# Optimization experiments

Hardware: AMD Instinct MI355X
Metric: run time of the kernel (lower is better)

Reference implementation:

```python
import jax, jax.numpy as jnp
import numpy as np

B, T, N, C = 32, 12, 1024, 2   # batch, lookback window, n_series, in_channels
D, H, K, OUT = 16, 64, 2, 12   # embedding_dim, rnn_units, cheb_k, out_dim (horizon)


def setup_inputs() -> dict:
    key = jax.random.key(0)
    ks = jax.random.split(key, 12)
    p = lambda k, sh, s=0.1: jax.random.normal(k, sh, dtype=jnp.float32) * s
    return {
        "source": jax.random.normal(ks[0], (B, T, N, C), dtype=jnp.float32),
        "node_emb": p(ks[1], (N, D), 0.3),
        # layer 0: dim_in = C + H
        "gate_w0": p(ks[2], (D, K, C + H, 2 * H)),
        "gate_b0": p(ks[3], (D, 2 * H)),
        "upd_w0": p(ks[4], (D, K, C + H, H)),
        "upd_b0": p(ks[5], (D, H)),
        # layer 1: dim_in = H + H
        "gate_w1": p(ks[6], (D, K, 2 * H, 2 * H)),
        "gate_b1": p(ks[7], (D, 2 * H)),
        "upd_w1": p(ks[8], (D, K, 2 * H, H)),
        "upd_b1": p(ks[9], (D, H)),
        # end_conv: Conv2d(1, OUT*out_channels, kernel=(1,H)) == linear over hidden dim
        "conv_w": p(ks[10], (OUT, H)),
        "conv_b": p(ks[11], (OUT,)),
    }


def _supports(node_emb):
    # softmax(relu(E E^T)) row-normalized adaptive adjacency; Chebyshev stack (K, N, N)
    A = jax.nn.softmax(jax.nn.relu(node_emb @ node_emb.T), axis=1)
    s = [jnp.eye(N, dtype=A.dtype), A]
    for _ in range(2, K):
        s.append(2.0 * A @ s[-1] - s[-2])
    return jnp.stack(s, axis=0)


def _gcn(x, node_emb, w_pool, b_pool, supports):
    # x: (B, N, Cin); per-node adaptive weights from pools
    w = jnp.einsum('nd,dkio->nkio', node_emb, w_pool)     # (N, K, Cin, Cout)
    b = node_emb @ b_pool                                 # (N, Cout)
    xg = jnp.einsum('knm,bmc->bnkc', supports, x)         # (B, N, K, Cin)
    return jnp.einsum('bnki,nkio->bno', xg, w) + b


def _layer(x_seq, node_emb, supports, gw, gb, uw, ub):
    # x_seq: (B, T, N, Cin) -> (B, T, N, H) via GRU-style AGCRN cell, scanned over T
    def step(state, x_t):
        inp = jnp.concatenate([x_t, state], axis=-1)
        zr = jax.nn.sigmoid(_gcn(inp, node_emb, gw, gb, supports))
        z, r = jnp.split(zr, 2, axis=-1)
        cand = jnp.concatenate([x_t, z * state], axis=-1)
        hc = jnp.tanh(_gcn(cand, node_emb, uw, ub, supports))
        h = r * state + (1.0 - r) * hc
        return h, h

    init = jnp.zeros((x_seq.shape[0], N, H), dtype=x_seq.dtype)
    _, hs = jax.lax.scan(step, init, jnp.swapaxes(x_seq, 0, 1))
    return jnp.swapaxes(hs, 0, 1)


def reference(source, node_emb, gate_w0, gate_b0, upd_w0, upd_b0,
              gate_w1, gate_b1, upd_w1, upd_b1, conv_w, conv_b,
              teacher_forcing_ratio=0):
    sup = _supports(node_emb)  # adaptive supports depend only on static node_emb
    h1 = _layer(source, node_emb, sup, gate_w0, gate_b0, upd_w0, upd_b0)
    h2 = _layer(h1, node_emb, sup, gate_w1, gate_b1, upd_w1, upd_b1)
    last = h2[:, -1]  # (B, N, H)
    # end_conv over hidden dim -> (B, OUT, N); out_channels==1 so squeeze folds away
    out = jnp.einsum('bnh,oh->bon', last, conv_w) + conv_b[None, :, None]
    return out
```

## Files before the change

kernel.cpp:

```cpp
#include <hip/hip_runtime.h>
#include <hip/hip_fp16.h>


typedef _Float16 f16x8 __attribute__((ext_vector_type(8)));
typedef _Float16 f16x2 __attribute__((ext_vector_type(2)));
typedef float f32x4 __attribute__((ext_vector_type(4)));

__global__ __launch_bounds__(256) void compute_A_kernel(const float* __restrict__ E,
                                                        __half* __restrict__ Ah) {
  int n = blockIdx.x;
  int tid = threadIdx.x;
  __shared__ float red[256];
  float en[16];
#pragma unroll
  for (int d = 0; d < 16; ++d) en[d] = E[n * 16 + d];
  float v[4];
#pragma unroll
  for (int q = 0; q < 4; ++q) {
    int m = tid + q * 256;
    const float* Em = E + m * 16;
    float dot = 0.f;
#pragma unroll
    for (int d = 0; d < 16; ++d) dot += en[d] * Em[d];
    v[q] = fmaxf(dot, 0.f);
  }
  float mx = fmaxf(fmaxf(v[0], v[1]), fmaxf(v[2], v[3]));
  red[tid] = mx; __syncthreads();
  for (int s = 128; s > 0; s >>= 1) { if (tid < s) red[tid] = fmaxf(red[tid], red[tid + s]); __syncthreads(); }
  mx = red[0];
  __syncthreads();
  float e[4], sum = 0.f;
#pragma unroll
  for (int q = 0; q < 4; ++q) { e[q] = expf(v[q] - mx); sum += e[q]; }
  red[tid] = sum; __syncthreads();
  for (int s = 128; s > 0; s >>= 1) { if (tid < s) red[tid] += red[tid + s]; __syncthreads(); }
  float inv = 1.f / red[0];
#pragma unroll
  for (int q = 0; q < 4; ++q) Ah[(size_t)n * 1024 + tid + q * 256] = __float2half(e[q] * inv);
}

__global__ void pool_transpose_all_kernel(const float* __restrict__ gw0, const float* __restrict__ uw0,
                                          const float* __restrict__ gw1, const float* __restrict__ uw1,
                                          float* __restrict__ poolT) {
  int t = blockIdx.x * 256 + threadIdx.x;
  if (t >= 1277952) return;
  const float* pool; int F, Fp, O, loc;
  if (t < 327680)       { pool = gw0; F = 66;  Fp = 80;  O = 128; loc = t; }
  else if (t < 491520)  { pool = uw0; F = 66;  Fp = 80;  O = 64;  loc = t - 327680; }
  else if (t < 1015808) { pool = gw1; F = 128; Fp = 128; O = 128; loc = t - 491520; }
  else                  { pool = uw1; F = 128; Fp = 128; O = 64;  loc = t - 1015808; }
  int KIp = 2 * Fp;
  int kip = loc % KIp;
  int rest = loc / KIp;
  int o = rest % O;
  int d = rest / O;
  int kk = (kip >= Fp) ? 1 : 0;
  int j = kip - kk * Fp;
  int i;
  if (F == Fp) i = j;
  else i = (j < 64) ? j + 2 : (j < 66 ? j - 64 : -1);
  poolT[t] = (i >= 0) ? pool[(((size_t)d * 2 + kk) * F + i) * O + o] : 0.f;
}

__global__ __launch_bounds__(256) void make_wt_all_kernel(
    const float* __restrict__ E, const float* __restrict__ poolT,
    __half* __restrict__ WtG0, __half* __restrict__ WtU0,
    __half* __restrict__ WtG1, __half* __restrict__ WtU1) {
  __shared__ float Es[64 * 17];
  __shared__ __align__(16) _Float16 wbuf[64][264];
  int bx = blockIdx.x;
  int o, O, KIp; const float* pt; __half* Wt;
  if (bx < 128)      { o = bx;       O = 128; KIp = 160; pt = poolT;           Wt = WtG0; }
  else if (bx < 192) { o = bx - 128; O = 64;  KIp = 160; pt = poolT + 327680;  Wt = WtU0; }
  else if (bx < 320) { o = bx - 192; O = 128; KIp = 256; pt = poolT + 491520;  Wt = WtG1; }
  else               { o = bx - 320; O = 64;  KIp = 256; pt = poolT + 1015808; Wt = WtU1; }
  int n0 = blockIdx.y * 64;
  {
    int nl = threadIdx.x >> 2, d0 = (threadIdx.x & 3) * 4;
    float4 v = *(const float4*)(E + (size_t)(n0 + nl) * 16 + d0);
    Es[nl * 17 + d0 + 0] = v.x; Es[nl * 17 + d0 + 1] = v.y;
    Es[nl * 17 + d0 + 2] = v.z; Es[nl * 17 + d0 + 3] = v.w;
  }
  __syncthreads();
  int nl = threadIdx.x & 63;
  int q = KIp >> 2;
  int ku = __builtin_amdgcn_readfirstlane((threadIdx.x >> 6) * q);
  float e[16];
#pragma unroll
  for (int d = 0; d < 16; ++d) e[d] = Es[nl * 17 + d];
  const float* pbase = pt + (size_t)o * KIp + ku;
  int strideOK = O * KIp;
  for (int kk = 0; kk < q; kk += 8) {
    float a[8] = {0.f, 0.f, 0.f, 0.f, 0.f, 0.f, 0.f, 0.f};
#pragma unroll
    for (int d = 0; d < 16; ++d) {
      const float* pd = pbase + (size_t)d * strideOK + kk;
#pragma unroll
      for (int j = 0; j < 8; ++j) a[j] = fmaf(e[d], pd[j], a[j]);
    }
    f16x8 pk;
#pragma unroll
    for (int j = 0; j < 8; ++j) pk[j] = (_Float16)a[j];
    *(f16x8*)&wbuf[nl][ku + kk] = pk;
  }
  __syncthreads();
  int chunks = KIp >> 3;
  int tot = 64 * chunks;
  for (int idx = threadIdx.x; idx < tot; idx += 256) {
    int nsub = idx / chunks;
    int pos = (idx - nsub * chunks) * 8;
    *(float4*)(Wt + ((size_t)(n0 + nsub) * O + o) * KIp + pos) = *(float4*)&wbuf[nsub][pos];
  }
}

__global__ void make_b_all_kernel(const float* __restrict__ E,
                                  const float* __restrict__ gb0, const float* __restrict__ ub0,
                                  const float* __restrict__ gb1, const float* __restrict__ ub1,
                                  float* __restrict__ Bg0, float* __restrict__ Bu0,
                                  float* __restrict__ Bg1, float* __restrict__ Bu1) {
  int tid = blockIdx.x * 256 + threadIdx.x;
  if (tid >= 1024 * 384) return;
  int n = tid / 384, c = tid - n * 384;
  const float* pool; float* outp; int O, o;
  if (c < 128)      { pool = gb0; outp = Bg0; O = 128; o = c; }
  else if (c < 192) { pool = ub0; outp = Bu0; O = 64;  o = c - 128; }
  else if (c < 320) { pool = gb1; outp = Bg1; O = 128; o = c - 192; }
  else              { pool = ub1; outp = Bu1; O = 64;  o = c - 320; }
  const float* En = E + n * 16;
  float a = 0.f;
#pragma unroll
  for (int d = 0; d < 16; ++d) a += En[d] * pool[d * O + o];
  outp[n * O + o] = a;
}

__global__ void zero_kernel(float* __restrict__ p, int count) {
  int i = blockIdx.x * 256 + threadIdx.x;
  if (i < count) p[i] = 0.f;
}

__global__ void build_x16_kernel(const float* __restrict__ src, __half* __restrict__ x16) {
  int bid = blockIdx.x; int t = bid >> 5, b = bid & 31;
  const float* s = src + (size_t)(b * 12 + t) * 2048;
  __half* dst = x16 + t * 64 + b * 2;
  for (int n = threadIdx.x; n < 1024; n += 256) {
    float2 v = *(const float2*)(s + n * 2);
    *(__half2*)(dst + (size_t)n * 768) = __floats2half2_rn(v.x, v.y);
  }
}

__global__ __launch_bounds__(256) void gemm_nt_kernel(
    const __half* __restrict__ Ahg, const __half* __restrict__ X0g,
    const __half* __restrict__ X1g, __half* __restrict__ Yg,
    int Nc, int cstride, int split) {
  __shared__ __align__(16) _Float16 As[64][72];
  __shared__ __align__(16) _Float16 Bs[64][80];
  const _Float16* __restrict__ Ah = (const _Float16*)Ahg;
  _Float16* __restrict__ Y = (_Float16*)Yg;
  int tid = threadIdx.x;
  int row0 = blockIdx.y * 64;
  int col0 = blockIdx.x * 64;
  const _Float16* __restrict__ Xsrc =
      (col0 < split) ? (const _Float16*)X0g : (const _Float16*)X1g;
  int colg = (col0 < split) ? col0 : col0 - split;
  int wave = tid >> 6, lane = tid & 63;
  int wm = wave & 1, wn = wave >> 1;
  int fm = lane & 15, fg = lane >> 4;

  int sr = tid >> 2, sc = (tid & 3) * 16;
  const _Float16* pa = Ah + (size_t)(row0 + sr) * 1024 + sc;
  int kp = tid & 31, cg = tid >> 5;
  const _Float16* pb0 = Xsrc + (size_t)(2 * kp) * cstride + colg + cg * 8;
  const _Float16* pb1 = pb0 + cstride;

  f16x8 ra0 = *(const f16x8*)(pa);
  f16x8 ra1 = *(const f16x8*)(pa + 8);
  f16x8 rb0 = *(const f16x8*)(pb0);
  f16x8 rb1 = *(const f16x8*)(pb1);

  int kk = 2 * kp;
  int kchunk = kp >> 2;
  int kin = kk & 7;
  f32x4 acc[2][2] = {};
  for (int k0 = 0; k0 < 1024; k0 += 64) {
    *(f16x8*)&As[sr][sc] = ra0;
    *(f16x8*)&As[sr][sc + 8] = ra1;
#pragma unroll
    for (int i = 0; i < 8; ++i) {
      int c = cg * 8 + i;
      f16x2 p; p[0] = rb0[i]; p[1] = rb1[i];
      int pos = ((kchunk ^ (c & 7)) << 3) + kin;
      *(f16x2*)&Bs[c][pos] = p;
    }
    __syncthreads();
    if (k0 + 64 < 1024) {
      ra0 = *(const f16x8*)(pa + k0 + 64);
      ra1 = *(const f16x8*)(pa + k0 + 72);
      rb0 = *(const f16x8*)(pb0 + (size_t)(k0 + 64) * cstride);
      rb1 = *(const f16x8*)(pb1 + (size_t)(k0 + 64) * cstride);
    }
#pragma unroll
    for (int kc = 0; kc < 2; ++kc) {
      int ck = kc * 4 + fg;
      f16x8 af[2], bf[2];
#pragma unroll
      for (int i = 0; i < 2; ++i)
        af[i] = *(const f16x8*)&As[wm * 32 + i * 16 + fm][kc * 32 + fg * 8];
#pragma unroll
      for (int j = 0; j < 2; ++j) {
        int cl = wn * 32 + j * 16 + fm;
        bf[j] = *(const f16x8*)&Bs[cl][(ck ^ (cl & 7)) << 3];
      }
#pragma unroll
      for (int i = 0; i < 2; ++i)
#pragma unroll
        for (int j = 0; j < 2; ++j)
          acc[i][j] = __builtin_amdgcn_mfma_f32_16x16x32_f16(af[i], bf[j], acc[i][j], 0, 0, 0);
    }
    __syncthreads();
  }
#pragma unroll
  for (int i = 0; i < 2; ++i) {
#pragma unroll
    for (int j = 0; j < 2; ++j) {
      int col = col0 + wn * 32 + j * 16 + fm;
      int rbase = row0 + wm * 32 + i * 16 + fg * 4;
#pragma unroll
      for (int r = 0; r < 4; ++r)
        Y[(size_t)(rbase + r) * Nc + col] = (_Float16)acc[i][j][r];
    }
  }
}

__global__ __launch_bounds__(256) void gate0_kernel(
    const __half* __restrict__ h16, const __half* __restrict__ YB,
    const float* __restrict__ src, const __half* __restrict__ Axt, int tstep,
    const __half* __restrict__ Wtg, const float* __restrict__ Bg,
    const float* __restrict__ h32, __half* __restrict__ zh, float* __restrict__ rbuf) {
  constexpr int KIP = 160, STRIDE = 168;
  __shared__ __align__(16) _Float16 Xs[32 * STRIDE];
  int n = blockIdx.x;
  int t = threadIdx.x;
#pragma unroll
  for (int u = 0; u < 2; ++u) {
    int idx = t + u * 256;
    int b = idx >> 4, part = (idx >> 3) & 1, ch = idx & 7;
    const _Float16* s = part ? (const _Float16*)YB + (size_t)n * 2048 + b * 64 + ch * 8
                             : (const _Float16*)h16 + (size_t)n * 2048 + b * 64 + ch * 8;
    *(f16x8*)&Xs[b * STRIDE + part * 80 + ch * 8] = *(const f16x8*)s;
  }
  if (t < 32) {
    int b = t;
    float2 xv = *(const float2*)(src + ((size_t)(b * 12 + tstep) * 1024 + n) * 2);
    Xs[b * STRIDE + 64] = (_Float16)xv.x;
    Xs[b * STRIDE + 65] = (_Float16)xv.y;
    const _Float16* ax = (const _Float16*)Axt + (size_t)n * 768 + tstep * 64 + b * 2;
    Xs[b * STRIDE + 144] = ax[0];
    Xs[b * STRIDE + 145] = ax[1];
  }
  for (int idx = t; idx < 896; idx += 256) {
    int b = idx / 28, jj = idx % 28;
    int col = (jj < 14) ? 66 + jj : 132 + jj;
    Xs[b * STRIDE + col] = (_Float16)0.f;
  }
  __syncthreads();
  int wave = t >> 6, lane = t & 63;
  int fm = lane & 15, fg = lane >> 4;
  f32x4 acc[2][2] = {};
  const _Float16* Wn = (const _Float16*)Wtg + ((size_t)n * 128 + wave * 32) * KIP;
#pragma unroll
  for (int kc = 0; kc < KIP / 32; ++kc) {
    f16x8 af[2], bf[2];
#pragma unroll
    for (int i = 0; i < 2; ++i)
      af[i] = *(const f16x8*)&Xs[(i * 16 + fm) * STRIDE + kc * 32 + fg * 8];
#pragma unroll
    for (int j = 0; j < 2; ++j)
      bf[j] = *(const f16x8*)(Wn + (size_t)(j * 16 + fm) * KIP + kc * 32 + fg * 8);
#pragma unroll
    for (int i = 0; i < 2; ++i)
#pragma unroll
      for (int j = 0; j < 2; ++j)
        acc[i][j] = __builtin_amdgcn_mfma_f32_16x16x32_f16(af[i], bf[j], acc[i][j], 0, 0, 0);
  }
  const float* Bn = Bg + n * 128;
#pragma unroll
  for (int j = 0; j < 2; ++j) {
    int o = wave * 32 + j * 16 + fm;
    float bias = Bn[o];
#pragma unroll
    for (int i = 0; i < 2; ++i)
#pragma unroll
      for (int r = 0; r < 4; ++r) {
        int b = i * 16 + fg * 4 + r;
        float s = 1.f / (1.f + __expf(-(acc[i][j][r] + bias)));
        size_t base = (size_t)n * 2048 + b * 64;
        if (o < 64) zh[base + o] = __float2half(s * h32[base + o]);
        else        rbuf[base + o - 64] = s;
      }
  }
}

__global__ __launch_bounds__(256) void upd0_kernel(
    const __half* __restrict__ zh, const __half* __restrict__ YA2,
    const float* __restrict__ src, const __half* __restrict__ Axt, int tstep,
    const __half* __restrict__ Wtg, const float* __restrict__ Bu,
    const float* __restrict__ rbuf, float* __restrict__ h32, __half* __restrict__ h16) {
  constexpr int KIP = 160, STRIDE = 168;
  __shared__ __align__(16) _Float16 Xs[32 * STRIDE];
  int n = blockIdx.x;
  int t = threadIdx.x;
#pragma unroll
  for (int u = 0; u < 2; ++u) {
    int idx = t + u * 256;
    int b = idx >> 4, part = (idx >> 3) & 1, ch = idx & 7;
    const _Float16* s = part ? (const _Float16*)YA2 + (size_t)n * 4096 + b * 64 + ch * 8
                             : (const _Float16*)zh + (size_t)n * 2048 + b * 64 + ch * 8;
    *(f16x8*)&Xs[b * STRIDE + part * 80 + ch * 8] = *(const f16x8*)s;
  }
  if (t < 32) {
    int b = t;
    float2 xv = *(const float2*)(src + ((size_t)(b * 12 + tstep) * 1024 + n) * 2);
    Xs[b * STRIDE + 64] = (_Float16)xv.x;
    Xs[b * STRIDE + 65] = (_Float16)xv.y;
    const _Float16* ax = (const _Float16*)Axt + (size_t)n * 768 + tstep * 64 + b * 2;
    Xs[b * STRIDE + 144] = ax[0];
    Xs[b * STRIDE + 145] = ax[1];
  }
  for (int idx = t; idx < 896; idx += 256) {
    int b = idx / 28, jj = idx % 28;
    int col = (jj < 14) ? 66 + jj : 132 + jj;
    Xs[b * STRIDE + col] = (_Float16)0.f;
  }
  __syncthreads();
  int wave = t >> 6, lane = t & 63;
  int fm = lane & 15, fg = lane >> 4;
  f32x4 acc[2] = {};
  const _Float16* Wn = (const _Float16*)Wtg + ((size_t)n * 64 + wave * 16) * KIP;
#pragma unroll
  for (int kc = 0; kc < KIP / 32; ++kc) {
    f16x8 bf = *(const f16x8*)(Wn + (size_t)fm * KIP + kc * 32 + fg * 8);
#pragma unroll
    for (int i = 0; i < 2; ++i) {
      f16x8 af = *(const f16x8*)&Xs[(i * 16 + fm) * STRIDE + kc * 32 + fg * 8];
      acc[i] = __builtin_amdgcn_mfma_f32_16x16x32_f16(af, bf, acc[i], 0, 0, 0);
    }
  }
  int o = wave * 16 + fm;
  float bias = Bu[n * 64 + o];
#pragma unroll
  for (int i = 0; i < 2; ++i)
#pragma unroll
    for (int r = 0; r < 4; ++r) {
      int b = i * 16 + fg * 4 + r;
      float x = acc[i][r] + bias;
      x = fminf(fmaxf(x, -15.f), 15.f);
      float e = __expf(2.f * x);
      float hc = (e - 1.f) / (e + 1.f);
      size_t base = (size_t)n * 2048 + b * 64;
      float rr = rbuf[base + o];
      float hnew = rr * h32[base + o] + (1.f - rr) * hc;
      h32[base + o] = hnew;
      h16[base + o] = __float2half(hnew);
    }
}

__global__ __launch_bounds__(256) void gate1_kernel(
    const __half* __restrict__ h1_16, const __half* __restrict__ h2_16,
    const __half* __restrict__ YB, const __half* __restrict__ YA2,
    const __half* __restrict__ Wtg, const float* __restrict__ Bg,
    const float* __restrict__ h32, __half* __restrict__ zh, float* __restrict__ rbuf) {
  constexpr int KIP = 256, STRIDE = 264;
  __shared__ __align__(16) _Float16 Xs[32 * STRIDE];
  int n = blockIdx.x;
  int t = threadIdx.x;
#pragma unroll
  for (int u = 0; u < 4; ++u) {
    int idx = t + u * 256;
    int b = idx >> 5, q = idx & 31;
    const _Float16* s;
    if (q < 8)       s = (const _Float16*)h1_16 + (size_t)n * 2048 + b * 64 + q * 8;
    else if (q < 16) s = (const _Float16*)h2_16 + (size_t)n * 2048 + b * 64 + (q - 8) * 8;
    else if (q < 24) s = (const _Float16*)YB + (size_t)n * 2048 + b * 64 + (q - 16) * 8;
    else             s = (const _Float16*)YA2 + (size_t)n * 4096 + 2048 + b * 64 + (q - 24) * 8;
    *(f16x8*)&Xs[b * STRIDE + q * 8] = *(const f16x8*)s;
  }
  __syncthreads();
  int wave = t >> 6, lane = t & 63;
  int fm = lane & 15, fg = lane >> 4;
  f32x4 acc[2][2] = {};
  const _Float16* Wn = (const _Float16*)Wtg + ((size_t)n * 128 + wave * 32) * KIP;
#pragma unroll
  for (int kc = 0; kc < KIP / 32; ++kc) {
    f16x8 af[2], bf[2];
#pragma unroll
    for (int i = 0; i < 2; ++i)
      af[i] = *(const f16x8*)&Xs[(i * 16 + fm) * STRIDE + kc * 32 + fg * 8];
#pragma unroll
    for (int j = 0; j < 2; ++j)
      bf[j] = *(const f16x8*)(Wn + (size_t)(j * 16 + fm) * KIP + kc * 32 + fg * 8);
#pragma unroll
    for (int i = 0; i < 2; ++i)
#pragma unroll
      for (int j = 0; j < 2; ++j)
        acc[i][j] = __builtin_amdgcn_mfma_f32_16x16x32_f16(af[i], bf[j], acc[i][j], 0, 0, 0);
  }
  const float* Bn = Bg + n * 128;
#pragma unroll
  for (int j = 0; j < 2; ++j) {
    int o = wave * 32 + j * 16 + fm;
    float bias = Bn[o];
#pragma unroll
    for (int i = 0; i < 2; ++i)
#pragma unroll
      for (int r = 0; r < 4; ++r) {
        int b = i * 16 + fg * 4 + r;
        float s = 1.f / (1.f + __expf(-(acc[i][j][r] + bias)));
        size_t base = (size_t)n * 2048 + b * 64;
        if (o < 64) zh[base + o] = __float2half(s * h32[base + o]);
        else        rbuf[base + o - 64] = s;
      }
  }
}

__global__ __launch_bounds__(256) void upd1_kernel(
    const __half* __restrict__ h1_16, const __half* __restrict__ zh,
    const __half* __restrict__ YB, const __half* __restrict__ YC,
    const __half* __restrict__ Wtg, const float* __restrict__ Bu,
    const float* __restrict__ rbuf, float* __restrict__ h32, __half* __restrict__ h16) {
  constexpr int KIP = 256, STRIDE = 264;
  __shared__ __align__(16) _Float16 Xs[32 * STRIDE];
  int n = blockIdx.x;
  int t = threadIdx.x;
#pragma unroll
  for (int u = 0; u < 4; ++u) {
    int idx = t + u * 256;
    int b = idx >> 5, q = idx & 31;
    const _Float16* s;
    if (q < 8)       s = (const _Float16*)h1_16 + (size_t)n * 2048 + b * 64 + q * 8;
    else if (q < 16) s = (const _Float16*)zh + (size_t)n * 2048 + b * 64 + (q - 8) * 8;
    else if (q < 24) s = (const _Float16*)YB + (size_t)n * 2048 + b * 64 + (q - 16) * 8;
    else             s = (const _Float16*)YC + (size_t)n * 2048 + b * 64 + (q - 24) * 8;
    *(f16x8*)&Xs[b * STRIDE + q * 8] = *(const f16x8*)s;
  }
  __syncthreads();
  int wave = t >> 6, lane = t & 63;
  int fm = lane & 15, fg = lane >> 4;
  f32x4 acc[2] = {};
  const _Float16* Wn = (const _Float16*)Wtg + ((size_t)n * 64 + wave * 16) * KIP;
#pragma unroll
  for (int kc = 0; kc < KIP / 32; ++kc) {
    f16x8 bf = *(const f16x8*)(Wn + (size_t)fm * KIP + kc * 32 + fg * 8);
#pragma unroll
    for (int i = 0; i < 2; ++i) {
      f16x8 af = *(const f16x8*)&Xs[(i * 16 + fm) * STRIDE + kc * 32 + fg * 8];
      acc[i] = __builtin_amdgcn_mfma_f32_16x16x32_f16(af, bf, acc[i], 0, 0, 0);
    }
  }
  int o = wave * 16 + fm;
  float bias = Bu[n * 64 + o];
#pragma unroll
  for (int i = 0; i < 2; ++i)
#pragma unroll
    for (int r = 0; r < 4; ++r) {
      int b = i * 16 + fg * 4 + r;
      float x = acc[i][r] + bias;
      x = fminf(fmaxf(x, -15.f), 15.f);
      float e = __expf(2.f * x);
      float hc = (e - 1.f) / (e + 1.f);
      size_t base = (size_t)n * 2048 + b * 64;
      float rr = rbuf[base + o];
      float hnew = rr * h32[base + o] + (1.f - rr) * hc;
      h32[base + o] = hnew;
      h16[base + o] = __float2half(hnew);
    }
}

__global__ void final_conv_kernel(const float* __restrict__ h2, const float* __restrict__ cw,
                                  const float* __restrict__ cb, float* __restrict__ out) {
  int tid = blockIdx.x * 256 + threadIdx.x;
  if (tid >= 32 * 1024) return;
  int n = tid & 1023, b = tid >> 10;
  const float* hp = h2 + ((size_t)n * 32 + b) * 64;
  float hv[64];
#pragma unroll
  for (int i = 0; i < 64; ++i) hv[i] = hp[i];
#pragma unroll
  for (int o = 0; o < 12; ++o) {
    float acc = cb[o];
#pragma unroll
    for (int i = 0; i < 64; ++i) acc += hv[i] * cw[o * 64 + i];
    out[((size_t)b * 12 + o) * 1024 + n] = acc;
  }
}

extern "C" void kernel_launch(void* const* d_in, const int* in_sizes, int n_in,
                              void* d_out, int out_size, void* d_ws, size_t ws_size,
                              hipStream_t stream) {
  const float* src = (const float*)d_in[0];
  const float* E   = (const float*)d_in[1];
  const float* gw0 = (const float*)d_in[2];
  const float* gb0 = (const float*)d_in[3];
  const float* uw0 = (const float*)d_in[4];
  const float* ub0 = (const float*)d_in[5];
  const float* gw1 = (const float*)d_in[6];
  const float* gb1 = (const float*)d_in[7];
  const float* uw1 = (const float*)d_in[8];
  const float* ub1 = (const float*)d_in[9];
  const float* cw  = (const float*)d_in[10];
  const float* cb  = (const float*)d_in[11];
  float* out = (float*)d_out;
  (void)in_sizes; (void)n_in; (void)out_size; (void)ws_size;

  char* base = (char*)d_ws;
  size_t off = 0;
  auto alloc = [&](size_t bytes) -> void* {
    void* p = base + off; off += (bytes + 511) & ~(size_t)511; return p;
  };
  __half* Ah   = (__half*)alloc((size_t)1024 * 1024 * 2);
  __half* WtG0 = (__half*)alloc((size_t)1024 * 128 * 160 * 2);
  __half* WtU0 = (__half*)alloc((size_t)1024 * 64 * 160 * 2);
  __half* WtG1 = (__half*)alloc((size_t)1024 * 128 * 256 * 2);
  __half* WtU1 = (__half*)alloc((size_t)1024 * 64 * 256 * 2);
  float*  Bg0  = (float*) alloc((size_t)1024 * 128 * 4);
  float*  Bu0  = (float*) alloc((size_t)1024 * 64 * 4);
  float*  Bg1  = (float*) alloc((size_t)1024 * 128 * 4);
  float*  Bu1  = (float*) alloc((size_t)1024 * 64 * 4);
  float*  h1_32 = (float*)alloc((size_t)1024 * 2048 * 4);
  float*  h2_32 = (float*)alloc((size_t)1024 * 2048 * 4);
  __half* h1_16 = (__half*)alloc((size_t)1024 * 2048 * 2);
  __half* h2_16 = (__half*)alloc((size_t)1024 * 2048 * 2);
  __half* YB   = (__half*)alloc((size_t)1024 * 2048 * 2);
  __half* zh   = (__half*)alloc((size_t)1024 * 2048 * 2);
  __half* YA2  = (__half*)alloc((size_t)1024 * 4096 * 2);
  __half* YC   = (__half*)alloc((size_t)1024 * 2048 * 2);
  __half* Axt  = (__half*)alloc((size_t)1024 * 768 * 2);
  float*  rbuf = (float*) alloc((size_t)1024 * 2048 * 4);
  float*  poolT = rbuf;
  __half* x16  = (__half*)(rbuf + (size_t)1310720);

  compute_A_kernel<<<1024, 256, 0, stream>>>(E, Ah);
  pool_transpose_all_kernel<<<(1277952 + 255) / 256, 256, 0, stream>>>(gw0, uw0, gw1, uw1, poolT);
  make_wt_all_kernel<<<dim3(384, 16), 256, 0, stream>>>(E, poolT, WtG0, WtU0, WtG1, WtU1);
  make_b_all_kernel<<<(1024 * 384 + 255) / 256, 256, 0, stream>>>(E, gb0, ub0, gb1, ub1,
                                                                  Bg0, Bu0, Bg1, Bu1);
  build_x16_kernel<<<384, 256, 0, stream>>>(src, x16);
  gemm_nt_kernel<<<dim3(12, 16), 256, 0, stream>>>(Ah, (__half*)x16, (__half*)x16, Axt,
                                                   768, 768, 768);
  zero_kernel<<<(7340032 + 255) / 256, 256, 0, stream>>>(h1_32, 7340032);

  for (int t = 0; t < 12; ++t) {
    gate0_kernel<<<1024, 256, 0, stream>>>(h1_16, YB, src, Axt, t, WtG0, Bg0, h1_32, zh, rbuf);
    gemm_nt_kernel<<<dim3(64, 16), 256, 0, stream>>>(Ah, zh, h2_16, YA2, 4096, 2048, 2048);
    upd0_kernel<<<1024, 256, 0, stream>>>(zh, YA2, src, Axt, t, WtU0, Bu0, rbuf, h1_32, h1_16);
    gemm_nt_kernel<<<dim3(32, 16), 256, 0, stream>>>(Ah, h1_16, h1_16, YB, 2048, 2048, 2048);
    gate1_kernel<<<1024, 256, 0, stream>>>(h1_16, h2_16, YB, YA2, WtG1, Bg1, h2_32, zh, rbuf);
    gemm_nt_kernel<<<dim3(32, 16), 256, 0, stream>>>(Ah, zh, zh, YC, 2048, 2048, 2048);
    upd1_kernel<<<1024, 256, 0, stream>>>(h1_16, zh, YB, YC, WtU1, Bu1, rbuf, h2_32, h2_16);
  }

  final_conv_kernel<<<(32 * 1024 + 255) / 256, 256, 0, stream>>>(h2_32, cw, cb, out);
}
```

Measured before the change: 1.523 ms.

## Compute per-node weights with MFMA and double K-tile depth in support GEMM

The per-node weight generation (E times weight pools) moves from scalar FP32 FMAs to an MFMA GEMM. E and the transposed pools are converted to fp16 and zero-padded along D to 32 first. Separately, the support GEMM now stages 128-wide K tiles per iteration instead of 64, which halves the barrier count and raises the bytes loaded per sync, at the cost of more LDS and registers. Computing the weights with fp16 inputs reduces their precision.

```diff
diff --git a/kernel.cpp b/kernel.cpp
--- a/kernel.cpp
+++ b/kernel.cpp
@@ -3,7 +3,7 @@
 
 
 typedef _Float16 f16x8 __attribute__((ext_vector_type(8)));
-typedef _Float16 f16x2 __attribute__((ext_vector_type(2)));
+typedef _Float16 f16x4 __attribute__((ext_vector_type(4)));
 typedef float f32x4 __attribute__((ext_vector_type(4)));
 
 __global__ __launch_bounds__(256) void compute_A_kernel(const float* __restrict__ E,
@@ -39,77 +39,81 @@
   for (int q = 0; q < 4; ++q) Ah[(size_t)n * 1024 + tid + q * 256] = __float2half(e[q] * inv);
 }
 
-__global__ void pool_transpose_all_kernel(const float* __restrict__ gw0, const float* __restrict__ uw0,
-                                          const float* __restrict__ gw1, const float* __restrict__ uw1,
-                                          float* __restrict__ poolT) {
+__global__ void build_e16_kernel(const float* __restrict__ E, __half* __restrict__ E16) {
   int t = blockIdx.x * 256 + threadIdx.x;
-  if (t >= 1277952) return;
+  if (t >= 1024 * 32) return;
+  int d = t & 31;
+  E16[t] = (d < 16) ? __float2half(E[(t >> 5) * 16 + d]) : __half(0);
+}
+
+__global__ void pool_t16_kernel(const float* __restrict__ gw0, const float* __restrict__ uw0,
+                                const float* __restrict__ gw1, const float* __restrict__ uw1,
+                                __half* __restrict__ poolT16) {
+  int t = blockIdx.x * 256 + threadIdx.x;
+  if (t >= 79872 * 32) return;
+  int d = t & 31, j = t >> 5;
+  if (d >= 16) { poolT16[t] = __half(0); return; }
   const float* pool; int F, Fp, O, loc;
-  if (t < 327680)       { pool = gw0; F = 66;  Fp = 80;  O = 128; loc = t; }
-  else if (t < 491520)  { pool = uw0; F = 66;  Fp = 80;  O = 64;  loc = t - 327680; }
-  else if (t < 1015808) { pool = gw1; F = 128; Fp = 128; O = 128; loc = t - 491520; }
-  else                  { pool = uw1; F = 128; Fp = 128; O = 64;  loc = t - 1015808; }
+  if (j < 20480)      { pool = gw0; F = 66;  Fp = 80;  O = 128; loc = j; }
+  else if (j < 30720) { pool = uw0; F = 66;  Fp = 80;  O = 64;  loc = j - 20480; }
+  else if (j < 63488) { pool = gw1; F = 128; Fp = 128; O = 128; loc = j - 30720; }
+  else                { pool = uw1; F = 128; Fp = 128; O = 64;  loc = j - 63488; }
   int KIp = 2 * Fp;
-  int kip = loc % KIp;
-  int rest = loc / KIp;
-  int o = rest % O;
-  int d = rest / O;
+  int o = loc / KIp, kip = loc - o * KIp;
   int kk = (kip >= Fp) ? 1 : 0;
-  int j = kip - kk * Fp;
+  int jj = kip - kk * Fp;
   int i;
-  if (F == Fp) i = j;
-  else i = (j < 64) ? j + 2 : (j < 66 ? j - 64 : -1);
-  poolT[t] = (i >= 0) ? pool[(((size_t)d * 2 + kk) * F + i) * O + o] : 0.f;
-}
-
-__global__ __launch_bounds__(256) void make_wt_all_kernel(
-    const float* __restrict__ E, const float* __restrict__ poolT,
+  if (F == Fp) i = jj;
+  else i = (jj < 64) ? jj + 2 : (jj < 66 ? jj - 64 : -1);
+  poolT16[t] = (i >= 0) ? __float2half(pool[(((size_t)d * 2 + kk) * F + i) * O + o]) : __half(0);
+}
+
+__global__ __launch_bounds__(256) void make_wt_mfma_kernel(
+    const __half* __restrict__ E16g, const __half* __restrict__ poolT16g,
     __half* __restrict__ WtG0, __half* __restrict__ WtU0,
     __half* __restrict__ WtG1, __half* __restrict__ WtU1) {
-  __shared__ float Es[64 * 17];
+  __shared__ __align__(16) _Float16 Es[64][40];
   __shared__ __align__(16) _Float16 wbuf[64][264];
+  const _Float16* E16 = (const _Float16*)E16g;
+  const _Float16* pT = (const _Float16*)poolT16g;
   int bx = blockIdx.x;
-  int o, O, KIp; const float* pt; __half* Wt;
-  if (bx < 128)      { o = bx;       O = 128; KIp = 160; pt = poolT;           Wt = WtG0; }
-  else if (bx < 192) { o = bx - 128; O = 64;  KIp = 160; pt = poolT + 327680;  Wt = WtU0; }
-  else if (bx < 320) { o = bx - 192; O = 128; KIp = 256; pt = poolT + 491520;  Wt = WtG1; }
-  else               { o = bx - 320; O = 64;  KIp = 256; pt = poolT + 1015808; Wt = WtU1; }
+  __half* Wt; int OK, jbase;
+  if (bx < 80)       { Wt = WtG0; OK = 128 * 160; jbase = bx * 256; }
+  else if (bx < 120) { Wt = WtU0; OK = 64 * 160;  jbase = (bx - 80) * 256; }
+  else if (bx < 248) { Wt = WtG1; OK = 128 * 256; jbase = (bx - 120) * 256; }
+  else               { Wt = WtU1; OK = 64 * 256;  jbase = (bx - 248) * 256; }
+  int jglob0 = bx * 256;
   int n0 = blockIdx.y * 64;
   {
-    int nl = threadIdx.x >> 2, d0 = (threadIdx.x & 3) * 4;
-    float4 v = *(const float4*)(E + (size_t)(n0 + nl) * 16 + d0);
-    Es[nl * 17 + d0 + 0] = v.x; Es[nl * 17 + d0 + 1] = v.y;
-    Es[nl * 17 + d0 + 2] = v.z; Es[nl * 17 + d0 + 3] = v.w;
-  }
-  __syncthreads();
-  int nl = threadIdx.x & 63;
-  int q = KIp >> 2;
-  int ku = __builtin_amdgcn_readfirstlane((threadIdx.x >> 6) * q);
-  float e[16];
-#pragma unroll
-  for (int d = 0; d < 16; ++d) e[d] = Es[nl * 17 + d];
-  const float* pbase = pt + (size_t)o * KIp + ku;
-  int strideOK = O * KIp;
-  for (int kk = 0; kk < q; kk += 8) {
-    float a[8] = {0.f, 0.f, 0.f, 0.f, 0.f, 0.f, 0.f, 0.f};
-#pragma unroll
-    for (int d = 0; d < 16; ++d) {
-      const float* pd = pbase + (size_t)d * strideOK + kk;
-#pragma unroll
-      for (int j = 0; j < 8; ++j) a[j] = fmaf(e[d], pd[j], a[j]);
-    }
-    f16x8 pk;
-#pragma unroll
-    for (int j = 0; j < 8; ++j) pk[j] = (_Float16)a[j];
-    *(f16x8*)&wbuf[nl][ku + kk] = pk;
-  }
-  __syncthreads();
-  int chunks = KIp >> 3;
-  int tot = 64 * chunks;
-  for (int idx = threadIdx.x; idx < tot; idx += 256) {
-    int nsub = idx / chunks;
-    int pos = (idx - nsub * chunks) * 8;
-    *(float4*)(Wt + ((size_t)(n0 + nsub) * O + o) * KIp + pos) = *(float4*)&wbuf[nsub][pos];
+    int r = threadIdx.x >> 2, ch = (threadIdx.x & 3) * 8;
+    *(f16x8*)&Es[r][ch] = *(const f16x8*)(E16 + (size_t)(n0 + r) * 32 + ch);
+  }
+  __syncthreads();
+  int wave = threadIdx.x >> 6, lane = threadIdx.x & 63;
+  int fm = lane & 15, fg = lane >> 4;
+  f16x8 af[4];
+#pragma unroll
+  for (int i = 0; i < 4; ++i) af[i] = *(const f16x8*)&Es[i * 16 + fm][fg * 8];
+  f32x4 acc[4][4] = {};
+#pragma unroll
+  for (int j = 0; j < 4; ++j) {
+    int jc = jglob0 + wave * 64 + j * 16 + fm;
+    f16x8 bf = *(const f16x8*)(pT + (size_t)jc * 32 + fg * 8);
+#pragma unroll
+    for (int i = 0; i < 4; ++i)
+      acc[i][j] = __builtin_amdgcn_mfma_f32_16x16x32_f16(af[i], bf, acc[i][j], 0, 0, 0);
+  }
+#pragma unroll
+  for (int i = 0; i < 4; ++i)
+#pragma unroll
+    for (int j = 0; j < 4; ++j)
+#pragma unroll
+      for (int r = 0; r < 4; ++r)
+        wbuf[i * 16 + fg * 4 + r][wave * 64 + j * 16 + fm] = (_Float16)acc[i][j][r];
+  __syncthreads();
+  for (int idx = threadIdx.x; idx < 64 * 32; idx += 256) {
+    int nsub = idx >> 5, pos = (idx & 31) * 8;
+    *(float4*)(Wt + (size_t)(n0 + nsub) * OK + jbase + pos) = *(float4*)&wbuf[nsub][pos];
   }
 }
 
@@ -152,8 +156,8 @@
     const __half* __restrict__ Ahg, const __half* __restrict__ X0g,
     const __half* __restrict__ X1g, __half* __restrict__ Yg,
     int Nc, int cstride, int split) {
-  __shared__ __align__(16) _Float16 As[64][72];
-  __shared__ __align__(16) _Float16 Bs[64][80];
+  __shared__ __align__(16) _Float16 As[64][136];
+  __shared__ __align__(16) _Float16 Bs[64][144];
   const _Float16* __restrict__ Ah = (const _Float16*)Ahg;
   _Float16* __restrict__ Y = (_Float16*)Yg;
   int tid = threadIdx.x;
@@ -166,40 +170,41 @@
   int wm = wave & 1, wn = wave >> 1;
   int fm = lane & 15, fg = lane >> 4;
 
-  int sr = tid >> 2, sc = (tid & 3) * 16;
+  int sr = tid >> 2, sc = (tid & 3) * 32;
   const _Float16* pa = Ah + (size_t)(row0 + sr) * 1024 + sc;
-  int kp = tid & 31, cg = tid >> 5;
-  const _Float16* pb0 = Xsrc + (size_t)(2 * kp) * cstride + colg + cg * 8;
-  const _Float16* pb1 = pb0 + cstride;
-
-  f16x8 ra0 = *(const f16x8*)(pa);
-  f16x8 ra1 = *(const f16x8*)(pa + 8);
-  f16x8 rb0 = *(const f16x8*)(pb0);
-  f16x8 rb1 = *(const f16x8*)(pb1);
-
-  int kk = 2 * kp;
-  int kchunk = kp >> 2;
-  int kin = kk & 7;
+  int kq = tid & 31, cg = tid >> 5;
+  int kb = 4 * kq;
+  const _Float16* pb = Xsrc + (size_t)kb * cstride + colg + cg * 8;
+  int chunk = kq >> 1;
+  int kin = (kq & 1) * 4;
+
+  f16x8 ra[4], rb[4];
+#pragma unroll
+  for (int c = 0; c < 4; ++c) ra[c] = *(const f16x8*)(pa + c * 8);
+#pragma unroll
+  for (int r = 0; r < 4; ++r) rb[r] = *(const f16x8*)(pb + (size_t)r * cstride);
+
   f32x4 acc[2][2] = {};
-  for (int k0 = 0; k0 < 1024; k0 += 64) {
-    *(f16x8*)&As[sr][sc] = ra0;
-    *(f16x8*)&As[sr][sc + 8] = ra1;
+  for (int k0 = 0; k0 < 1024; k0 += 128) {
+#pragma unroll
+    for (int c = 0; c < 4; ++c) *(f16x8*)&As[sr][sc + c * 8] = ra[c];
 #pragma unroll
     for (int i = 0; i < 8; ++i) {
       int c = cg * 8 + i;
-      f16x2 p; p[0] = rb0[i]; p[1] = rb1[i];
-      int pos = ((kchunk ^ (c & 7)) << 3) + kin;
-      *(f16x2*)&Bs[c][pos] = p;
+      f16x4 p;
+      p[0] = rb[0][i]; p[1] = rb[1][i]; p[2] = rb[2][i]; p[3] = rb[3][i];
+      *(f16x4*)&Bs[c][((chunk ^ (c & 7)) << 3) + kin] = p;
     }
     __syncthreads();
-    if (k0 + 64 < 1024) {
-      ra0 = *(const f16x8*)(pa + k0 + 64);
-      ra1 = *(const f16x8*)(pa + k0 + 72);
-      rb0 = *(const f16x8*)(pb0 + (size_t)(k0 + 64) * cstride);
-      rb1 = *(const f16x8*)(pb1 + (size_t)(k0 + 64) * cstride);
-    }
-#pragma unroll
-    for (int kc = 0; kc < 2; ++kc) {
+    if (k0 + 128 < 1024) {
+#pragma unroll
+      for (int c = 0; c < 4; ++c) ra[c] = *(const f16x8*)(pa + k0 + 128 + c * 8);
+#pragma unroll
+      for (int r = 0; r < 4; ++r)
+        rb[r] = *(const f16x8*)(pb + (size_t)(k0 + 128 + r) * cstride);
+    }
+#pragma unroll
+    for (int kc = 0; kc < 4; ++kc) {
       int ck = kc * 4 + fg;
       f16x8 af[2], bf[2];
 #pragma unroll
@@ -535,12 +540,14 @@
   __half* YC   = (__half*)alloc((size_t)1024 * 2048 * 2);
   __half* Axt  = (__half*)alloc((size_t)1024 * 768 * 2);
   float*  rbuf = (float*) alloc((size_t)1024 * 2048 * 4);
-  float*  poolT = rbuf;
-  __half* x16  = (__half*)(rbuf + (size_t)1310720);
+  __half* poolT16 = (__half*)rbuf;
+  __half* E16  = poolT16 + (size_t)79872 * 32;
+  __half* x16  = E16 + (size_t)1024 * 32;
 
   compute_A_kernel<<<1024, 256, 0, stream>>>(E, Ah);
-  pool_transpose_all_kernel<<<(1277952 + 255) / 256, 256, 0, stream>>>(gw0, uw0, gw1, uw1, poolT);
-  make_wt_all_kernel<<<dim3(384, 16), 256, 0, stream>>>(E, poolT, WtG0, WtU0, WtG1, WtU1);
+  build_e16_kernel<<<(1024 * 32 + 255) / 256, 256, 0, stream>>>(E, E16);
+  pool_t16_kernel<<<(79872 * 32 + 255) / 256, 256, 0, stream>>>(gw0, uw0, gw1, uw1, poolT16);
+  make_wt_mfma_kernel<<<dim3(312, 16), 256, 0, stream>>>(E16, poolT16, WtG0, WtU0, WtG1, WtU1);
   make_b_all_kernel<<<(1024 * 384 + 255) / 256, 256, 0, stream>>>(E, gb0, ub0, gb1, ub1,
                                                                   Bg0, Bu0, Bg1, Bu1);
   build_x16_kernel<<<384, 256, 0, stream>>>(src, x16);
```

New measurement: 1.516 ms. About the same (-0.4%).
